# Optimization experiments

Hardware: AMD Instinct MI355X
Metric: run time of the kernel (lower is better)

Reference implementation:

```python
import jax, jax.numpy as jnp
import numpy as np

CHAR_DIM = 96
COLOR_DIM = 16
GLYPH_DIM = CHAR_DIM * COLOR_DIM  # 1536 bounded id space
CHAR_EMB = 16
COLOR_EMB = 4
GLYPH_EMB = CHAR_EMB + COLOR_EMB  # 20
HID = 32
MAX_LEN = 64


def setup_inputs() -> dict:
    key = jax.random.key(0)
    ks = jax.random.split(key, 8)
    B, H, W = 4096, 21, 79
    glyph_chars = jax.random.randint(ks[0], (B, H, W), 0, CHAR_DIM)
    glyph_colors = jax.random.randint(ks[1], (B, H, W), 0, COLOR_DIM)
    # embedding tables (row CHAR_DIM / COLOR_DIM is the padding row)
    char_table = jax.random.normal(ks[2], (CHAR_DIM + 1, CHAR_EMB), jnp.float32) * 0.1
    col_table = jax.random.normal(ks[3], (COLOR_DIM + 1, COLOR_EMB), jnp.float32) * 0.1
    s = 1.0 / np.sqrt(HID)
    Wih = jax.random.uniform(ks[4], (HID, GLYPH_EMB), jnp.float32, -s, s)
    Whh = jax.random.uniform(ks[5], (HID, HID), jnp.float32, -s, s)
    bih = jax.random.uniform(ks[6], (HID,), jnp.float32, -s, s)
    bhh = jax.random.uniform(ks[7], (HID,), jnp.float32, -s, s)
    return dict(glyph_chars=glyph_chars, glyph_colors=glyph_colors,
                char_table=char_table, col_table=col_table,
                Wih=Wih, Whh=Whh, bih=bih, bhh=bhh)


def reference(glyph_chars, glyph_colors, char_table, col_table, Wih, Whh, bih, bhh):
    B = glyph_chars.shape[0]
    # combined glyph id in the bounded [0, GLYPH_DIM) space
    ids = (glyph_chars * COLOR_DIM + glyph_colors).reshape(B, -1)  # [B, H*W]
    # batched fixed-size histogram over the bounded id space (replaces per-sample torch.unique)
    counts = jnp.zeros((B, GLYPH_DIM), jnp.int32).at[jnp.arange(B)[:, None], ids].add(1)
    present = counts > 0  # [B, GLYPH_DIM]
    # sorted unique ids (ascending == lexicographic over (char,color)); absent ids pushed to GLYPH_DIM
    sorted_ids = jnp.sort(jnp.where(present, jnp.arange(GLYPH_DIM), GLYPH_DIM), axis=-1)[:, :MAX_LEN]
    is_pad = sorted_ids >= GLYPH_DIM
    char_bag = jnp.where(is_pad, CHAR_DIM, sorted_ids // COLOR_DIM)   # pad -> CHAR_DIM row
    color_bag = jnp.where(is_pad, COLOR_DIM, sorted_ids % COLOR_DIM)  # pad -> COLOR_DIM row
    bag = jnp.stack([char_bag, color_bag], axis=-1)  # [B, MAX_LEN, 2]
    lengths = jnp.minimum(present.sum(-1), MAX_LEN)  # [B]
    emb = jnp.concatenate([char_table[char_bag], col_table[color_bag]], axis=-1)  # [B, MAX_LEN, 20]
    # vanilla tanh RNN over the packed (variable-length) bag; keep hidden at last valid step
    def step(h, inp):
        x_t, t = inp  # x_t: [B, 20]
        h_new = jnp.tanh(x_t @ Wih.T + bih + h @ Whh.T + bhh)
        h = jnp.where((t < lengths)[:, None], h_new, h)
        return h, None
    h0 = jnp.zeros((B, HID), emb.dtype)
    h, _ = jax.lax.scan(step, h0, (emb.transpose(1, 0, 2), jnp.arange(MAX_LEN)))
    return h, emb, bag
```

## Files before the change

kernel.cpp:

```cpp
#include <hip/hip_runtime.h>
#include <hip/hip_bf16.h>

#define HW        1659
#define GLYPH_DIM 1536
#define NBL       8
#define THREADS   256
#define XSTRIDE   2568

typedef _Float16 half8 __attribute__((ext_vector_type(8)));
typedef float    f32x4 __attribute__((ext_vector_type(4)));

__device__ __forceinline__ float tanh_f(float x) {
    float e = __expf(x + x);
    return fmaf(-2.0f, __builtin_amdgcn_rcpf(e + 1.0f), 1.0f);
}

__device__ __forceinline__ unsigned int pk(float a, float b) {
    return __builtin_bit_cast(unsigned int, __builtin_amdgcn_cvt_pkrtz(a, b));
}

__device__ __forceinline__ half8 h8(unsigned int a, unsigned int b,
                                    unsigned int c, unsigned int d) {
    uint4 u = make_uint4(a, b, c, d);
    return __builtin_bit_cast(half8, u);
}

__global__ __launch_bounds__(THREADS, 4) void glyph_fused(
    const int* __restrict__ gchar, const int* __restrict__ gcol,
    const float* __restrict__ ctab, const float* __restrict__ ktab,
    const float* __restrict__ Wih, const float* __restrict__ Whh,
    const float* __restrict__ bih, const float* __restrict__ bhh,
    float* __restrict__ out_h, float* __restrict__ out_emb,
    float* __restrict__ out_bag)
{
    __shared__ unsigned int   mask[NBL][48];
    __shared__ unsigned short ids[NBL][64];
    __shared__ int            lens[NBL];
    __shared__ __align__(16) unsigned char xfrag[NBL * XSTRIDE];

    const int tid = threadIdx.x;
    const int b0  = blockIdx.x * NBL;

    const int n = tid & 15, g = (tid >> 4) & 3;
    half8 wihA0, wihA1, whhA0, whhA1;
    f32x4 bias0 = {0, 0, 0, 0}, bias1 = {0, 0, 0, 0};
    if (tid < 64) {
        #pragma unroll
        for (int j = 0; j < 8; ++j) {
            int k = (j < 4) ? (4 * g + j) : (12 + 4 * g + j);
            wihA0[j] = (_Float16)((k < 20) ? Wih[n * 20 + k] : 0.0f);
            wihA1[j] = (_Float16)((k < 20) ? Wih[(n + 16) * 20 + k] : 0.0f);
            whhA0[j] = (_Float16)Whh[n * 32 + k];
            whhA1[j] = (_Float16)Whh[(n + 16) * 32 + k];
        }
        #pragma unroll
        for (int i = 0; i < 4; ++i) {
            bias0[i] = bih[4 * g + i] + bhh[4 * g + i];
            bias1[i] = bih[16 + 4 * g + i] + bhh[16 + 4 * g + i];
        }
    }

    for (int w = tid; w < NBL * 48; w += THREADS)
        ((unsigned int*)mask)[w] = 0u;
    __syncthreads();

    const int4* cp = (const int4*)(gchar + (long)b0 * HW);
    const int4* kp = (const int4*)(gcol  + (long)b0 * HW);
    const int n4 = (NBL * HW) / 4;
    for (int idx = tid; idx < n4; idx += THREADS) {
        int4 c = cp[idx];
        int4 k = kp[idx];
        int gg  = idx * 4;
        int bl0 = gg / HW;
        int rem = gg - bl0 * HW;
        int bl1 = bl0 + ((rem + 1) >= HW);
        int bl2 = bl0 + ((rem + 2) >= HW);
        int bl3 = bl0 + ((rem + 3) >= HW);
        int id0 = c.x * 16 + k.x;
        int id1 = c.y * 16 + k.y;
        int id2 = c.z * 16 + k.z;
        int id3 = c.w * 16 + k.w;
        atomicOr(&mask[bl0][id0 >> 5], 1u << (id0 & 31));
        atomicOr(&mask[bl1][id1 >> 5], 1u << (id1 & 31));
        atomicOr(&mask[bl2][id2 >> 5], 1u << (id2 & 31));
        atomicOr(&mask[bl3][id3 >> 5], 1u << (id3 & 31));
    }
    __syncthreads();

    {
        const int bl  = tid >> 5;
        const int l32 = tid & 31;
        unsigned long long m = 0ull;
        if (l32 < 24)
            m = ((unsigned long long)mask[bl][2 * l32 + 1] << 32) |
                (unsigned long long)mask[bl][2 * l32];
        int cnt  = __popcll(m);
        int incl = cnt;
        #pragma unroll
        for (int d = 1; d < 32; d <<= 1) {
            int nb = __shfl_up(incl, d, 32);
            if (l32 >= d) incl += nb;
        }
        int excl  = incl - cnt;
        int total = __shfl(incl, 31, 32);
        if (l32 == 0) lens[bl] = min(total, 64);
        ids[bl][l32]      = GLYPH_DIM;
        ids[bl][l32 + 32] = GLYPH_DIM;
        unsigned long long mm = m;
        int r = excl;
        while (mm != 0ull && r < 64) {
            int bit = __builtin_ctzll(mm);
            ids[bl][r] = (unsigned short)(l32 * 64 + bit);
            ++r;
            mm &= (mm - 1ull);
        }
    }
    __syncthreads();

    for (int e = tid; e < NBL * 64; e += THREADS) {
        int nb = e >> 6, r = e & 63;
        int id = ids[nb][r];
        int ch = id >> 4;
        int co = (id >= GLYPH_DIM) ? 16 : (id & 15);
        const float4* crow = (const float4*)(ctab + ch * 16);
        float4 c0 = crow[0], c1 = crow[1], c2 = crow[2], c3 = crow[3];
        float4 k0 = *(const float4*)(ktab + co * 4);
        float* gp = out_emb + ((long)(b0 + nb) * 64 + r) * 20;
        *(float4*)(gp + 0)  = c0;
        *(float4*)(gp + 4)  = c1;
        *(float4*)(gp + 8)  = c2;
        *(float4*)(gp + 12) = c3;
        *(float4*)(gp + 16) = k0;
        *(float2*)(out_bag + ((long)(b0 + nb) * 64 + r) * 2) =
            make_float2((float)ch, (float)co);
        unsigned char* xp = &xfrag[nb * XSTRIDE + r * 40];
        *(uint2*)(xp + 0)  = make_uint2(pk(c0.x, c0.y), pk(c0.z, c0.w));
        *(uint2*)(xp + 8)  = make_uint2(pk(c1.x, c1.y), pk(c1.z, c1.w));
        *(uint2*)(xp + 16) = make_uint2(pk(c2.x, c2.y), pk(c2.z, c2.w));
        *(uint2*)(xp + 24) = make_uint2(pk(c3.x, c3.y), pk(c3.z, c3.w));
        *(uint2*)(xp + 32) = make_uint2(pk(k0.x, k0.y), pk(k0.z, k0.w));
    }
    __syncthreads();

    if (tid < 64) {
        const int nc  = n & (NBL - 1);
        const int len = lens[nc];
        const unsigned char* xb = &xfrag[nc * XSTRIDE];
        f32x4 d0 = {0, 0, 0, 0}, d1 = {0, 0, 0, 0};
        #pragma unroll 4
        for (int t = 0; t < 64; ++t) {
            const unsigned char* xp = xb + t * 40;
            uint2 lo = *(const uint2*)(xp + 8 * g);
            uint2 hi = (g == 0) ? *(const uint2*)(xp + 32) : make_uint2(0u, 0u);
            half8 xB = h8(lo.x, lo.y, hi.x, hi.y);
            f32x4 a0 = __builtin_amdgcn_mfma_f32_16x16x32_f16(wihA0, xB, bias0, 0, 0, 0);
            f32x4 a1 = __builtin_amdgcn_mfma_f32_16x16x32_f16(wihA1, xB, bias1, 0, 0, 0);
            half8 hB = h8(pk(d0[0], d0[1]), pk(d0[2], d0[3]),
                          pk(d1[0], d1[1]), pk(d1[2], d1[3]));
            a0 = __builtin_amdgcn_mfma_f32_16x16x32_f16(whhA0, hB, a0, 0, 0, 0);
            a1 = __builtin_amdgcn_mfma_f32_16x16x32_f16(whhA1, hB, a1, 0, 0, 0);
            bool upd = (t < len);
            #pragma unroll
            for (int i = 0; i < 4; ++i) {
                float h0 = tanh_f(a0[i]);
                float h1 = tanh_f(a1[i]);
                d0[i] = upd ? h0 : d0[i];
                d1[i] = upd ? h1 : d1[i];
            }
        }
        if (n < NBL) {
            float* op = out_h + (long)(b0 + n) * 32;
            #pragma unroll
            for (int i = 0; i < 4; ++i) {
                op[4 * g + i]      = d0[i];
                op[16 + 4 * g + i] = d1[i];
            }
        }
    }
}

extern "C" void kernel_launch(void* const* d_in, const int* in_sizes, int n_in,
                              void* d_out, int out_size, void* d_ws, size_t ws_size,
                              hipStream_t stream) {
    const int* gchar = (const int*)d_in[0];
    const int* gcol  = (const int*)d_in[1];
    const float* ctab = (const float*)d_in[2];
    const float* ktab = (const float*)d_in[3];
    const float* Wih  = (const float*)d_in[4];
    const float* Whh  = (const float*)d_in[5];
    const float* bih  = (const float*)d_in[6];
    const float* bhh  = (const float*)d_in[7];

    const int B = in_sizes[0] / HW;
    float* out_h   = (float*)d_out;
    float* out_emb = out_h + (long)B * 32;
    float* out_bag = out_emb + (long)B * 64 * 20;

    glyph_fused<<<B / NBL, THREADS, 0, stream>>>(
        gchar, gcol, ctab, ktab, Wih, Whh, bih, bhh, out_h, out_emb, out_bag);
}
```

Measured before the change: 37.54 us.

## Precompute input projection across all warps and fill MFMA columns with 16 samples

Raises the block to 16 samples and 1024 threads so the 16-column MFMA in the recurrence is fully used instead of duplicating 8 samples. The input projection Wih·x+bias for all 64 timesteps is computed in parallel by all 16 waves and stored as fp16 in LDS. This leaves only the Whh MFMAs on the serial recurrence path, with the next step's precomputed value prefetched one iteration ahead. The tradeoffs are fewer blocks and lower occupancy with large blocks, extra fp16 rounding of the precomputed projection, and launch_bounds(THREADS,4) now asking for 4 blocks of 1024 threads.

```diff
diff --git a/kernel.cpp b/kernel.cpp
--- a/kernel.cpp
+++ b/kernel.cpp
@@ -3,12 +3,12 @@
 
 #define HW        1659
 #define GLYPH_DIM 1536
-#define NBL       8
-#define THREADS   256
-#define XSTRIDE   2568
-
-typedef _Float16 half8 __attribute__((ext_vector_type(8)));
-typedef float    f32x4 __attribute__((ext_vector_type(4)));
+#define NBL       16
+#define THREADS   1024
+
+typedef _Float16 half8  __attribute__((ext_vector_type(8)));
+typedef _Float16 half2v __attribute__((ext_vector_type(2)));
+typedef float    f32x4  __attribute__((ext_vector_type(4)));
 
 __device__ __forceinline__ float tanh_f(float x) {
     float e = __expf(x + x);
@@ -36,32 +36,27 @@
     __shared__ unsigned int   mask[NBL][48];
     __shared__ unsigned short ids[NBL][64];
     __shared__ int            lens[NBL];
-    __shared__ __align__(16) unsigned char xfrag[NBL * XSTRIDE];
+    __shared__ uint4          P_lds[64][64];
 
     const int tid = threadIdx.x;
     const int b0  = blockIdx.x * NBL;
-
-    const int n = tid & 15, g = (tid >> 4) & 3;
-    half8 wihA0, wihA1, whhA0, whhA1;
-    f32x4 bias0 = {0, 0, 0, 0}, bias1 = {0, 0, 0, 0};
-    if (tid < 64) {
-        #pragma unroll
-        for (int j = 0; j < 8; ++j) {
-            int k = (j < 4) ? (4 * g + j) : (12 + 4 * g + j);
-            wihA0[j] = (_Float16)((k < 20) ? Wih[n * 20 + k] : 0.0f);
-            wihA1[j] = (_Float16)((k < 20) ? Wih[(n + 16) * 20 + k] : 0.0f);
-            whhA0[j] = (_Float16)Whh[n * 32 + k];
-            whhA1[j] = (_Float16)Whh[(n + 16) * 32 + k];
-        }
-        #pragma unroll
-        for (int i = 0; i < 4; ++i) {
-            bias0[i] = bih[4 * g + i] + bhh[4 * g + i];
-            bias1[i] = bih[16 + 4 * g + i] + bhh[16 + 4 * g + i];
-        }
-    }
-
-    for (int w = tid; w < NBL * 48; w += THREADS)
-        ((unsigned int*)mask)[w] = 0u;
+    const int n   = tid & 15, g = (tid >> 4) & 3;
+
+    half8 wihA0, wihA1;
+    f32x4 bias0, bias1;
+    #pragma unroll
+    for (int j = 0; j < 8; ++j) {
+        int k = (j < 4) ? (4 * g + j) : (12 + 4 * g + j);
+        wihA0[j] = (_Float16)((k < 20) ? Wih[n * 20 + k] : 0.0f);
+        wihA1[j] = (_Float16)((k < 20) ? Wih[(n + 16) * 20 + k] : 0.0f);
+    }
+    #pragma unroll
+    for (int i = 0; i < 4; ++i) {
+        bias0[i] = bih[4 * g + i] + bhh[4 * g + i];
+        bias1[i] = bih[16 + 4 * g + i] + bhh[16 + 4 * g + i];
+    }
+
+    if (tid < NBL * 48) ((unsigned int*)mask)[tid] = 0u;
     __syncthreads();
 
     const int4* cp = (const int4*)(gchar + (long)b0 * HW);
@@ -87,7 +82,7 @@
     }
     __syncthreads();
 
-    {
+    if (tid < NBL * 32) {
         const int bl  = tid >> 5;
         const int l32 = tid & 31;
         unsigned long long m = 0ull;
@@ -117,8 +112,8 @@
     }
     __syncthreads();
 
-    for (int e = tid; e < NBL * 64; e += THREADS) {
-        int nb = e >> 6, r = e & 63;
+    {
+        const int nb = tid >> 6, r = tid & 63;
         int id = ids[nb][r];
         int ch = id >> 4;
         int co = (id >= GLYPH_DIM) ? 16 : (id & 15);
@@ -133,32 +128,50 @@
         *(float4*)(gp + 16) = k0;
         *(float2*)(out_bag + ((long)(b0 + nb) * 64 + r) * 2) =
             make_float2((float)ch, (float)co);
-        unsigned char* xp = &xfrag[nb * XSTRIDE + r * 40];
-        *(uint2*)(xp + 0)  = make_uint2(pk(c0.x, c0.y), pk(c0.z, c0.w));
-        *(uint2*)(xp + 8)  = make_uint2(pk(c1.x, c1.y), pk(c1.z, c1.w));
-        *(uint2*)(xp + 16) = make_uint2(pk(c2.x, c2.y), pk(c2.z, c2.w));
-        *(uint2*)(xp + 24) = make_uint2(pk(c3.x, c3.y), pk(c3.z, c3.w));
-        *(uint2*)(xp + 32) = make_uint2(pk(k0.x, k0.y), pk(k0.z, k0.w));
+    }
+
+    {
+        const int w = tid >> 6;
+        #pragma unroll
+        for (int i = 0; i < 4; ++i) {
+            int t  = 4 * w + i;
+            int id = ids[n][t];
+            int ch = id >> 4;
+            int co = (id >= GLYPH_DIM) ? 16 : (id & 15);
+            float4 q1 = *(const float4*)(ctab + ch * 16 + 4 * g);
+            float4 q2 = (g == 0) ? *(const float4*)(ktab + co * 4)
+                                 : make_float4(0, 0, 0, 0);
+            half8 xB = h8(pk(q1.x, q1.y), pk(q1.z, q1.w),
+                          pk(q2.x, q2.y), pk(q2.z, q2.w));
+            f32x4 P0 = __builtin_amdgcn_mfma_f32_16x16x32_f16(wihA0, xB, bias0, 0, 0, 0);
+            f32x4 P1 = __builtin_amdgcn_mfma_f32_16x16x32_f16(wihA1, xB, bias1, 0, 0, 0);
+            P_lds[t][tid & 63] = make_uint4(pk(P0[0], P0[1]), pk(P0[2], P0[3]),
+                                            pk(P1[0], P1[1]), pk(P1[2], P1[3]));
+        }
     }
     __syncthreads();
 
     if (tid < 64) {
-        const int nc  = n & (NBL - 1);
-        const int len = lens[nc];
-        const unsigned char* xb = &xfrag[nc * XSTRIDE];
+        half8 whhA0, whhA1;
+        #pragma unroll
+        for (int j = 0; j < 8; ++j) {
+            int k = (j < 4) ? (4 * g + j) : (12 + 4 * g + j);
+            whhA0[j] = (_Float16)Whh[n * 32 + k];
+            whhA1[j] = (_Float16)Whh[(n + 16) * 32 + k];
+        }
+        const int len = lens[n];
+        uint4 pc = P_lds[0][tid];
         f32x4 d0 = {0, 0, 0, 0}, d1 = {0, 0, 0, 0};
-        #pragma unroll 4
         for (int t = 0; t < 64; ++t) {
-            const unsigned char* xp = xb + t * 40;
-            uint2 lo = *(const uint2*)(xp + 8 * g);
-            uint2 hi = (g == 0) ? *(const uint2*)(xp + 32) : make_uint2(0u, 0u);
-            half8 xB = h8(lo.x, lo.y, hi.x, hi.y);
-            f32x4 a0 = __builtin_amdgcn_mfma_f32_16x16x32_f16(wihA0, xB, bias0, 0, 0, 0);
-            f32x4 a1 = __builtin_amdgcn_mfma_f32_16x16x32_f16(wihA1, xB, bias1, 0, 0, 0);
+            uint4 pn = P_lds[(t < 63) ? t + 1 : 63][tid];
+            half8 pf = __builtin_bit_cast(half8, pc);
+            f32x4 c0, c1;
+            #pragma unroll
+            for (int i = 0; i < 4; ++i) { c0[i] = (float)pf[i]; c1[i] = (float)pf[4 + i]; }
             half8 hB = h8(pk(d0[0], d0[1]), pk(d0[2], d0[3]),
                           pk(d1[0], d1[1]), pk(d1[2], d1[3]));
-            a0 = __builtin_amdgcn_mfma_f32_16x16x32_f16(whhA0, hB, a0, 0, 0, 0);
-            a1 = __builtin_amdgcn_mfma_f32_16x16x32_f16(whhA1, hB, a1, 0, 0, 0);
+            f32x4 a0 = __builtin_amdgcn_mfma_f32_16x16x32_f16(whhA0, hB, c0, 0, 0, 0);
+            f32x4 a1 = __builtin_amdgcn_mfma_f32_16x16x32_f16(whhA1, hB, c1, 0, 0, 0);
             bool upd = (t < len);
             #pragma unroll
             for (int i = 0; i < 4; ++i) {
@@ -167,14 +180,13 @@
                 d0[i] = upd ? h0 : d0[i];
                 d1[i] = upd ? h1 : d1[i];
             }
-        }
-        if (n < NBL) {
-            float* op = out_h + (long)(b0 + n) * 32;
-            #pragma unroll
-            for (int i = 0; i < 4; ++i) {
-                op[4 * g + i]      = d0[i];
-                op[16 + 4 * g + i] = d1[i];
-            }
+            pc = pn;
+        }
+        float* op = out_h + (long)(b0 + n) * 32;
+        #pragma unroll
+        for (int i = 0; i < 4; ++i) {
+            op[4 * g + i]      = d0[i];
+            op[16 + 4 * g + i] = d1[i];
         }
     }
 }
```

Result: slower. 39.51 us (+5.3%).
